# Performance work log

Hardware: AMD Instinct MI355X
Metric: run time of the kernel (lower is better)

Reference implementation:

```python
import jax, jax.numpy as jnp
import numpy as np

B, N, C, H = 8, 4096, 768, 8


def setup_inputs() -> dict:
    key = jax.random.key(0)
    k1, k2, k3 = jax.random.split(key, 3)
    x = jax.random.normal(k1, (B, N, C), dtype=jnp.float32)
    W_qkv = jax.random.normal(k2, (C, 3 * C), dtype=jnp.float32) * 0.02
    W_proj = jax.random.normal(k3, (C, C), dtype=jnp.float32) * 0.02
    b_proj = jnp.zeros((C,), dtype=jnp.float32)
    temp = jnp.ones((H, 1, 1), dtype=jnp.float32)
    return {"x": x, "W_qkv": W_qkv, "W_proj": W_proj, "b_proj": b_proj, "temp": temp}


def reference(x, W_qkv, W_proj, b_proj, temp):
    b, n, c = x.shape
    h = temp.shape[0]
    d = c // h
    # qkv: [B,N,3C] -> [B,N,H,D,3]  (matches tf.reshape split order)
    qkv = (x @ W_qkv).reshape(b, n, h, d, 3)
    q, k, v = qkv[..., 0], qkv[..., 1], qkv[..., 2]
    # L2-normalize along the patch axis (axis=1), as tf.linalg.normalize
    q = q / jnp.linalg.norm(q, axis=1, keepdims=True)
    k = k / jnp.linalg.norm(k, axis=1, keepdims=True)
    # channel-wise (cross-covariance) attention: [B,H,D,D]
    attn = jnp.einsum('bnhd,bnhe->bhde', q, k) * temp
    attn = jax.nn.softmax(attn, axis=-1)
    # apply to v and fold heads back: [B,N,C]
    y = jnp.einsum('bhde,bnhe->bnhd', attn, v).reshape(b, n, c)
    return y @ W_proj + b_proj
```

## Files before the change

kernel.cpp:

```cpp
#include <hip/hip_runtime.h>

typedef __attribute__((ext_vector_type(8))) short short8;
typedef __attribute__((ext_vector_type(4))) float f32x4;

__device__ inline unsigned short f2b(float f) {
  unsigned int u = __builtin_bit_cast(unsigned int, f);
  u = (u + 0x7FFFu + ((u >> 16) & 1u)) >> 16;
  return (unsigned short)u;
}
__device__ inline float b2f(unsigned short s) {
  unsigned int u = ((unsigned int)s) << 16;
  return __builtin_bit_cast(float, u);
}

__device__ inline void async16(const void* g, void* l) {
  __builtin_amdgcn_global_load_lds((__attribute__((address_space(1))) void*)(g),
                                   (__attribute__((address_space(3))) void*)(l), 16, 0, 0);
}

__global__ void cvt_x(const float4* __restrict__ x, ushort4* __restrict__ xb, int n4) {
  int i = blockIdx.x * blockDim.x + threadIdx.x;
  int stride = gridDim.x * blockDim.x;
  for (; i < n4; i += stride) {
    float4 v = x[i];
    ushort4 o;
    o.x = f2b(v.x); o.y = f2b(v.y); o.z = f2b(v.z); o.w = f2b(v.w);
    xb[i] = o;
  }
}

__global__ __launch_bounds__(256) void t_wqkv(const float* __restrict__ W, unsigned short* __restrict__ Wt) {
  __shared__ float tile[32][33];
  int j0 = blockIdx.x * 32, c0 = blockIdx.y * 32;
  int tx = threadIdx.x & 31, ty = threadIdx.x >> 5;
#pragma unroll
  for (int r = 0; r < 32; r += 8)
    tile[ty + r][tx] = W[(size_t)(c0 + ty + r) * 2304 + j0 + tx];
  __syncthreads();
#pragma unroll
  for (int r = 0; r < 32; r += 8) {
    int j = j0 + ty + r;
    int h = j / 288, rem = j - h * 288;
    int d = rem / 3, s = rem - d * 3;
    int jj = s * 768 + h * 96 + d;
    Wt[(size_t)jj * 768 + c0 + tx] = f2b(tile[tx][ty + r]);
  }
}

__global__ __launch_bounds__(256) void t_wproj(const float* __restrict__ W, unsigned short* __restrict__ Wt) {
  __shared__ float tile[32][33];
  int j0 = blockIdx.x * 32, c0 = blockIdx.y * 32;
  int tx = threadIdx.x & 31, ty = threadIdx.x >> 5;
#pragma unroll
  for (int r = 0; r < 32; r += 8)
    tile[ty + r][tx] = W[(size_t)(c0 + ty + r) * 768 + j0 + tx];
  __syncthreads();
#pragma unroll
  for (int r = 0; r < 32; r += 8)
    Wt[(size_t)(j0 + ty + r) * 768 + c0 + tx] = f2b(tile[tx][ty + r]);
}

__global__ __launch_bounds__(512, 2) void gemm_qkv(
    const unsigned short* __restrict__ A, const unsigned short* __restrict__ Bt,
    unsigned short* __restrict__ Q, unsigned short* __restrict__ Kd, unsigned short* __restrict__ V) {
  extern __shared__ __align__(16) unsigned short smem[];
  const int tid = threadIdx.x;
  const int wave = tid >> 6, lane = tid & 63;
  const int mlane = lane & 15, quad = lane >> 4;
  const int m0 = blockIdx.x * 256, n0 = blockIdx.y * 256;
  const int wm = (wave >> 2) * 128;
  const int wn = (wave & 3) * 64;

  f32x4 acc[8][4] = {};

  auto stage = [&](int kt, int c) {
    const int k0 = kt * 64;
    unsigned short* As_c = smem + c * 32768;
    unsigned short* Bs_c = As_c + 16384;
#pragma unroll
    for (int i = 0; i < 4; ++i) {
      int ebase = i * 512 + (wave << 6);
      int e = ebase + lane;
      int row = e >> 3, slot = e & 7;
      async16(A + (size_t)(m0 + row) * 768 + k0 + slot * 8, As_c + (size_t)ebase * 8);
      async16(Bt + (size_t)(n0 + row) * 768 + k0 + slot * 8, Bs_c + (size_t)ebase * 8);
    }
  };

  stage(0, 0);
  stage(1, 1);
  asm volatile("s_waitcnt vmcnt(8)" ::: "memory");
  __builtin_amdgcn_s_barrier();

#pragma unroll 1
  for (int t = 0; t < 12; ++t) {
    const int c = t & 1;
    const unsigned short* As_c = smem + c * 32768;
    const unsigned short* Bs_c = As_c + 16384;

    short8 af[2][2][4];
    short8 bf[2][4];
#pragma unroll
    for (int mh = 0; mh < 2; ++mh)
#pragma unroll
      for (int kk = 0; kk < 2; ++kk)
#pragma unroll
        for (int f = 0; f < 4; ++f)
          af[mh][kk][f] = *(const short8*)&As_c[(wm + mh * 64 + f * 16 + mlane) * 64 + kk * 32 + quad * 8];
#pragma unroll
    for (int kk = 0; kk < 2; ++kk)
#pragma unroll
      for (int j = 0; j < 4; ++j)
        bf[kk][j] = *(const short8*)&Bs_c[(wn + j * 16 + mlane) * 64 + kk * 32 + quad * 8];

    if (t < 10) {
      asm volatile("s_waitcnt lgkmcnt(0)" ::: "memory");
      __builtin_amdgcn_sched_barrier(0);
      __builtin_amdgcn_s_barrier();
      stage(t + 2, c);
    }

    __builtin_amdgcn_s_setprio(1);
#pragma unroll
    for (int kk = 0; kk < 2; ++kk)
#pragma unroll
      for (int mh = 0; mh < 2; ++mh)
#pragma unroll
        for (int f = 0; f < 4; ++f)
#pragma unroll
          for (int j = 0; j < 4; ++j)
            acc[mh * 4 + f][j] =
                __builtin_amdgcn_mfma_f32_16x16x32_bf16(af[mh][kk][f], bf[kk][j], acc[mh * 4 + f][j], 0, 0, 0);
    __builtin_amdgcn_s_setprio(0);

    if (t < 10) {
      asm volatile("s_waitcnt vmcnt(8)" ::: "memory");
      __builtin_amdgcn_s_barrier();
    } else if (t == 10) {
      asm volatile("s_waitcnt vmcnt(0)" ::: "memory");
      __builtin_amdgcn_s_barrier();
    }
  }

  const int bb = m0 >> 12;
  const int nb = (m0 & 4095) + wm + quad * 4;
#pragma unroll
  for (int j = 0; j < 4; ++j) {
    int jj = n0 + wn + j * 16 + mlane;
    int s = jj / 768;
    int hd = jj - s * 768;
    int h = hd / 96;
    int d = hd - h * 96;
    unsigned short* dst = (s == 0) ? Q : (s == 1) ? Kd : V;
    size_t colbase = ((size_t)(bb * 8 + h) * 4096) * 96 + d;
#pragma unroll
    for (int mf = 0; mf < 8; ++mf) {
      int n = nb + (mf >> 2) * 64 + (mf & 3) * 16;
#pragma unroll
      for (int r = 0; r < 4; ++r)
        dst[colbase + (size_t)(n + r) * 96] = f2b(acc[mf][j][r]);
    }
  }
}

__global__ __launch_bounds__(256) void attn_partial(
    const unsigned short* __restrict__ Q, const unsigned short* __restrict__ Kd,
    float* __restrict__ Spart, float* __restrict__ sq, float* __restrict__ sk) {
  int chunk = blockIdx.x;
  int bh = blockIdx.y;
  __shared__ __align__(16) unsigned short QT[96 * 72];
  __shared__ __align__(16) unsigned short KT[96 * 72];
  int t = threadIdx.x;
  int wave = t >> 6, lane = t & 63, mlane = lane & 15, quad = lane >> 4;
  int wrow = (wave >> 1) * 48, wcol = (wave & 1) * 48;
  f32x4 acc[3][3] = {};
  const unsigned int* qp = (const unsigned int*)(Q + (size_t)bh * 4096 * 96);
  const unsigned int* kp = (const unsigned int*)(Kd + (size_t)bh * 4096 * 96);
  int c = t % 48, rg = t / 48;
  int nbeg = chunk * 256;
  float aq0 = 0.f, aq1 = 0.f, ak0 = 0.f, ak1 = 0.f;
  for (int n0 = nbeg; n0 < nbeg + 256; n0 += 64) {
    __syncthreads();
    if (rg < 5) {
      for (int n = rg; n < 64; n += 5) {
        unsigned int qv = qp[(size_t)(n0 + n) * 48 + c];
        unsigned int kv = kp[(size_t)(n0 + n) * 48 + c];
        QT[(2 * c) * 72 + n] = (unsigned short)(qv & 0xffff);
        QT[(2 * c + 1) * 72 + n] = (unsigned short)(qv >> 16);
        KT[(2 * c) * 72 + n] = (unsigned short)(kv & 0xffff);
        KT[(2 * c + 1) * 72 + n] = (unsigned short)(kv >> 16);
        float q0 = b2f((unsigned short)(qv & 0xffff)), q1 = b2f((unsigned short)(qv >> 16));
        float k0 = b2f((unsigned short)(kv & 0xffff)), k1 = b2f((unsigned short)(kv >> 16));
        aq0 += q0 * q0; aq1 += q1 * q1; ak0 += k0 * k0; ak1 += k1 * k1;
      }
    }
    __syncthreads();
#pragma unroll
    for (int kk = 0; kk < 64; kk += 32) {
      short8 a[3], bf[3];
#pragma unroll
      for (int f = 0; f < 3; ++f)
        a[f] = *(const short8*)&QT[(wrow + f * 16 + mlane) * 72 + kk + quad * 8];
#pragma unroll
      for (int f = 0; f < 3; ++f)
        bf[f] = *(const short8*)&KT[(wcol + f * 16 + mlane) * 72 + kk + quad * 8];
#pragma unroll
      for (int i = 0; i < 3; ++i)
#pragma unroll
        for (int j = 0; j < 3; ++j)
          acc[i][j] = __builtin_amdgcn_mfma_f32_16x16x32_bf16(a[i], bf[j], acc[i][j], 0, 0, 0);
    }
  }
  if (rg < 5) {
    atomicAdd(&sq[bh * 96 + 2 * c], aq0);
    atomicAdd(&sq[bh * 96 + 2 * c + 1], aq1);
    atomicAdd(&sk[bh * 96 + 2 * c], ak0);
    atomicAdd(&sk[bh * 96 + 2 * c + 1], ak1);
  }
  float* dst = Spart + ((size_t)bh * 16 + chunk) * 9216;
#pragma unroll
  for (int i = 0; i < 3; ++i)
#pragma unroll
    for (int j = 0; j < 3; ++j)
#pragma unroll
      for (int r = 0; r < 4; ++r)
        dst[(wrow + i * 16 + quad * 4 + r) * 96 + wcol + j * 16 + mlane] = acc[i][j][r];
}

__global__ __launch_bounds__(256) void attn_finalize(
    const float* __restrict__ Spart, const float* __restrict__ sq,
    const float* __restrict__ sk, const float* __restrict__ temp,
    unsigned short* __restrict__ P) {
  int bh = blockIdx.x, h = bh & 7;
  __shared__ float S[9216];
  __shared__ float rk[96], rq[96];
  int t = threadIdx.x;
  const float* base = Spart + (size_t)bh * 16 * 9216;
  if (t < 96) {
    rk[t] = rsqrtf(sk[bh * 96 + t]);
    rq[t] = rsqrtf(sq[bh * 96 + t]) * temp[h];
  }
  __syncthreads();
  for (int i = t; i < 9216; i += 256) {
    float s = 0.f;
#pragma unroll
    for (int c2 = 0; c2 < 16; ++c2) s += base[(size_t)c2 * 9216 + i];
    int d = i / 96, e = i - d * 96;
    S[i] = s * rq[d] * rk[e];
  }
  __syncthreads();
  if (t < 96) {
    int d = t;
    float mx = -1e30f;
    for (int e = 0; e < 96; ++e) mx = fmaxf(mx, S[d * 96 + e]);
    float sum = 0.f;
    for (int e = 0; e < 96; ++e) {
      float v = expf(S[d * 96 + e] - mx);
      S[d * 96 + e] = v;
      sum += v;
    }
    float inv = 1.0f / sum;
    for (int e = 0; e < 96; ++e)
      P[(size_t)bh * 9216 + d * 96 + e] = f2b(S[d * 96 + e] * inv);
  }
}

__global__ __launch_bounds__(256) void gemm_pv(
    const unsigned short* __restrict__ V, const unsigned short* __restrict__ P,
    unsigned short* __restrict__ y) {
  int bh = blockIdx.y;
  int b = bh >> 3, h = bh & 7;
  int m0 = blockIdx.x * 128;
  int t = threadIdx.x, wave = t >> 6, lane = t & 63, mlane = lane & 15, quad = lane >> 4;
  const unsigned short* Vb = V + (size_t)bh * 4096 * 96;
  const unsigned short* Pb = P + (size_t)bh * 9216;
  f32x4 acc[2][6] = {};
#pragma unroll
  for (int kk = 0; kk < 96; kk += 32) {
    short8 a[2], bfr[6];
#pragma unroll
    for (int i = 0; i < 2; ++i)
      a[i] = *(const short8*)&Vb[(size_t)(m0 + wave * 32 + i * 16 + mlane) * 96 + kk + quad * 8];
#pragma unroll
    for (int j = 0; j < 6; ++j)
      bfr[j] = *(const short8*)&Pb[(j * 16 + mlane) * 96 + kk + quad * 8];
#pragma unroll
    for (int i = 0; i < 2; ++i)
#pragma unroll
      for (int j = 0; j < 6; ++j)
        acc[i][j] = __builtin_amdgcn_mfma_f32_16x16x32_bf16(a[i], bfr[j], acc[i][j], 0, 0, 0);
  }
#pragma unroll
  for (int i = 0; i < 2; ++i) {
    int n = m0 + wave * 32 + i * 16 + quad * 4;
#pragma unroll
    for (int j = 0; j < 6; ++j) {
      int d = j * 16 + mlane;
#pragma unroll
      for (int r = 0; r < 4; ++r)
        y[((size_t)b * 4096 + n + r) * 768 + h * 96 + d] = f2b(acc[i][j][r]);
    }
  }
}

__global__ __launch_bounds__(256) void gemm_proj(
    const unsigned short* __restrict__ A, const unsigned short* __restrict__ Bt,
    const float* __restrict__ bias, float* __restrict__ out) {
  __shared__ __align__(16) unsigned short As[128 * 64];
  __shared__ __align__(16) unsigned short Bs[128 * 64];
  const int tid = threadIdx.x;
  const int wave = tid >> 6, lane = tid & 63;
  const int mlane = lane & 15, quad = lane >> 4;
  const int m0 = blockIdx.x * 128, n0 = blockIdx.y * 128;
  const int wm = (wave >> 1) * 64, wn = (wave & 1) * 64;
  f32x4 acc[4][4] = {};
  for (int k0 = 0; k0 < 768; k0 += 64) {
    __syncthreads();
#pragma unroll
    for (int t = 0; t < 4; ++t) {
      int ebase = t * 256 + (wave << 6);
      int e = ebase + lane;
      int row = e >> 3, c8 = e & 7;
      async16(A + (size_t)(m0 + row) * 768 + k0 + c8 * 8, As + ebase * 8);
      async16(Bt + (size_t)(n0 + row) * 768 + k0 + c8 * 8, Bs + ebase * 8);
    }
    __syncthreads();
#pragma unroll
    for (int kk = 0; kk < 64; kk += 32) {
      short8 a[4], b[4];
#pragma unroll
      for (int f = 0; f < 4; ++f)
        a[f] = *(const short8*)&As[(wm + f * 16 + mlane) * 64 + kk + quad * 8];
#pragma unroll
      for (int f = 0; f < 4; ++f)
        b[f] = *(const short8*)&Bs[(wn + f * 16 + mlane) * 64 + kk + quad * 8];
#pragma unroll
      for (int i = 0; i < 4; ++i)
#pragma unroll
        for (int j = 0; j < 4; ++j)
          acc[i][j] = __builtin_amdgcn_mfma_f32_16x16x32_bf16(a[i], b[j], acc[i][j], 0, 0, 0);
    }
  }
#pragma unroll
  for (int fn = 0; fn < 4; ++fn) {
    int col = n0 + wn + fn * 16 + mlane;
    float bv = bias[col];
#pragma unroll
    for (int fm = 0; fm < 4; ++fm) {
      int m = m0 + wm + fm * 16 + quad * 4;
#pragma unroll
      for (int r = 0; r < 4; ++r)
        out[(size_t)(m + r) * 768 + col] = acc[fm][fn][r] + bv;
    }
  }
}

extern "C" void kernel_launch(void* const* d_in, const int* in_sizes, int n_in,
                              void* d_out, int out_size, void* d_ws, size_t ws_size,
                              hipStream_t stream) {
  const float* x = (const float*)d_in[0];
  const float* Wqkv = (const float*)d_in[1];
  const float* Wproj = (const float*)d_in[2];
  const float* bias = (const float*)d_in[3];
  const float* temp = (const float*)d_in[4];
  float* out = (float*)d_out;

  char* ws = (char*)d_ws;
  size_t off = 0;
  auto alloc = [&](size_t bytes) -> void* {
    void* p = ws + off;
    off += (bytes + 255) & ~(size_t)255;
    return p;
  };
  unsigned short* xb = (unsigned short*)alloc(32768ull * 768 * 2);
  unsigned short* Wtq = (unsigned short*)alloc(2304ull * 768 * 2);
  unsigned short* Wtp = (unsigned short*)alloc(768ull * 768 * 2);
  unsigned short* Q = (unsigned short*)alloc(64ull * 4096 * 96 * 2);
  unsigned short* Kd = (unsigned short*)alloc(64ull * 4096 * 96 * 2);
  unsigned short* V = (unsigned short*)alloc(64ull * 4096 * 96 * 2);
  float* sq = (float*)alloc(64 * 96 * 4);
  float* sk = (float*)alloc(64 * 96 * 4);
  unsigned short* P = (unsigned short*)alloc(64ull * 9216 * 2);
  (void)off; (void)ws_size; (void)in_sizes; (void)n_in; (void)out_size;

  float* Spart = out;

  static bool attr_set = false;
  if (!attr_set) {
    hipFuncSetAttribute((const void*)gemm_qkv, hipFuncAttributeMaxDynamicSharedMemorySize, 131072);
    attr_set = true;
  }

  cvt_x<<<4096, 256, 0, stream>>>((const float4*)x, (ushort4*)xb, 32768 * 768 / 4);
  t_wqkv<<<dim3(72, 24), 256, 0, stream>>>(Wqkv, Wtq);
  t_wproj<<<dim3(24, 24), 256, 0, stream>>>(Wproj, Wtp);
  hipMemsetAsync(sq, 0, 64 * 96 * 4, stream);
  hipMemsetAsync(sk, 0, 64 * 96 * 4, stream);
  gemm_qkv<<<dim3(128, 9), 512, 131072, stream>>>(xb, Wtq, Q, Kd, V);
  attn_partial<<<dim3(16, 64), 256, 0, stream>>>(Q, Kd, Spart, sq, sk);
  attn_finalize<<<64, 256, 0, stream>>>(Spart, sq, sk, temp, P);
  gemm_pv<<<dim3(32, 64), 256, 0, stream>>>(V, P, xb );
  gemm_proj<<<dim3(256, 6), 256, 0, stream>>>(xb , Wtp, bias, out);
}
```

Measured before the change: 552.3 us.

## Swizzle LDS tiles and interleave fragment loads with MFMA in QKV GEMM

The QKV GEMM now stores A and B tiles in LDS with an XOR swizzle on the 16-byte slot index, which is meant to remove bank conflicts on the fragment reads. The main loop is split into four phases, each loading a subset of fragments and then issuing 16 MFMAs, with barriers in between. This lowers register pressure and lets LDS reads overlap with other waves' math. The next-stage prefetch is issued before the last MFMA phase, and the epilogue store loop is reordered. The extra barriers add sync overhead.

```diff
diff --git a/kernel.cpp b/kernel.cpp
--- a/kernel.cpp
+++ b/kernel.cpp
@@ -68,97 +68,140 @@
   const int wave = tid >> 6, lane = tid & 63;
   const int mlane = lane & 15, quad = lane >> 4;
   const int m0 = blockIdx.x * 256, n0 = blockIdx.y * 256;
-  const int wm = (wave >> 2) * 128;
+  const int ah = wave >> 2;
+  const int wm = ah * 128;
   const int wn = (wave & 3) * 64;
+  const int bh = wn >> 7;
+  const int bl = wn & 64;
 
   f32x4 acc[8][4] = {};
 
   auto stage = [&](int kt, int c) {
     const int k0 = kt * 64;
-    unsigned short* As_c = smem + c * 32768;
-    unsigned short* Bs_c = As_c + 16384;
-#pragma unroll
-    for (int i = 0; i < 4; ++i) {
-      int ebase = i * 512 + (wave << 6);
-      int e = ebase + lane;
-      int row = e >> 3, slot = e & 7;
-      async16(A + (size_t)(m0 + row) * 768 + k0 + slot * 8, As_c + (size_t)ebase * 8);
-      async16(Bt + (size_t)(n0 + row) * 768 + k0 + slot * 8, Bs_c + (size_t)ebase * 8);
-    }
+#pragma unroll
+    for (int h = 0; h < 4; ++h) {
+      const unsigned short* src = (h < 2) ? A : Bt;
+      const int rbase = ((h < 2) ? m0 : n0) + (h & 1) * 128;
+      unsigned short* ldsbase = smem + c * 32768 + h * 8192;
+#pragma unroll
+      for (int i = 0; i < 2; ++i) {
+        int ebase = i * 512 + (wave << 6);
+        int e = ebase + lane;
+        int row = e >> 3;
+        int slot = (e & 7) ^ (row & 7);
+        async16(src + (size_t)(rbase + row) * 768 + k0 + slot * 8, ldsbase + ebase * 8);
+      }
+    }
+  };
+
+  auto rdA = [&](const unsigned short* base, int mh, int kk, int f) -> short8 {
+    int r = mh * 64 + f * 16 + mlane;
+    return *(const short8*)&base[r * 64 + ((kk * 32 + quad * 8) ^ ((r & 7) << 3))];
+  };
+  auto rdB = [&](const unsigned short* base, int kk, int j) -> short8 {
+    int r = bl + j * 16 + mlane;
+    return *(const short8*)&base[r * 64 + ((kk * 32 + quad * 8) ^ ((r & 7) << 3))];
   };
 
   stage(0, 0);
   stage(1, 1);
   asm volatile("s_waitcnt vmcnt(8)" ::: "memory");
+  __builtin_amdgcn_sched_barrier(0);
   __builtin_amdgcn_s_barrier();
 
 #pragma unroll 1
   for (int t = 0; t < 12; ++t) {
     const int c = t & 1;
-    const unsigned short* As_c = smem + c * 32768;
-    const unsigned short* Bs_c = As_c + 16384;
-
-    short8 af[2][2][4];
-    short8 bf[2][4];
-#pragma unroll
-    for (int mh = 0; mh < 2; ++mh)
-#pragma unroll
-      for (int kk = 0; kk < 2; ++kk)
-#pragma unroll
-        for (int f = 0; f < 4; ++f)
-          af[mh][kk][f] = *(const short8*)&As_c[(wm + mh * 64 + f * 16 + mlane) * 64 + kk * 32 + quad * 8];
-#pragma unroll
-    for (int kk = 0; kk < 2; ++kk)
+    const unsigned short* Abase = smem + c * 32768 + ah * 8192;
+    const unsigned short* Bbase = smem + c * 32768 + 16384 + bh * 8192;
+    short8 a0[4], a1[4], b0[4], b1[4];
+
+#pragma unroll
+    for (int j = 0; j < 4; ++j) b0[j] = rdB(Bbase, 0, j);
+#pragma unroll
+    for (int f = 0; f < 4; ++f) a0[f] = rdA(Abase, 0, 0, f);
+    asm volatile("s_waitcnt lgkmcnt(0)" ::: "memory");
+    __builtin_amdgcn_sched_barrier(0);
+    __builtin_amdgcn_s_setprio(1);
+#pragma unroll
+    for (int f = 0; f < 4; ++f)
 #pragma unroll
       for (int j = 0; j < 4; ++j)
-        bf[kk][j] = *(const short8*)&Bs_c[(wn + j * 16 + mlane) * 64 + kk * 32 + quad * 8];
-
-    if (t < 10) {
-      asm volatile("s_waitcnt lgkmcnt(0)" ::: "memory");
-      __builtin_amdgcn_sched_barrier(0);
-      __builtin_amdgcn_s_barrier();
-      stage(t + 2, c);
-    }
-
+        acc[f][j] = __builtin_amdgcn_mfma_f32_16x16x32_bf16(a0[f], b0[j], acc[f][j], 0, 0, 0);
+    __builtin_amdgcn_s_setprio(0);
+    __builtin_amdgcn_s_barrier();
+
+#pragma unroll
+    for (int f = 0; f < 4; ++f) a1[f] = rdA(Abase, 1, 0, f);
+#pragma unroll
+    for (int j = 0; j < 4; ++j) b1[j] = rdB(Bbase, 1, j);
+    asm volatile("s_waitcnt lgkmcnt(0)" ::: "memory");
+    __builtin_amdgcn_sched_barrier(0);
     __builtin_amdgcn_s_setprio(1);
 #pragma unroll
-    for (int kk = 0; kk < 2; ++kk)
-#pragma unroll
-      for (int mh = 0; mh < 2; ++mh)
-#pragma unroll
-        for (int f = 0; f < 4; ++f)
-#pragma unroll
-          for (int j = 0; j < 4; ++j)
-            acc[mh * 4 + f][j] =
-                __builtin_amdgcn_mfma_f32_16x16x32_bf16(af[mh][kk][f], bf[kk][j], acc[mh * 4 + f][j], 0, 0, 0);
+    for (int f = 0; f < 4; ++f)
+#pragma unroll
+      for (int j = 0; j < 4; ++j)
+        acc[4 + f][j] = __builtin_amdgcn_mfma_f32_16x16x32_bf16(a1[f], b0[j], acc[4 + f][j], 0, 0, 0);
     __builtin_amdgcn_s_setprio(0);
-
+    __builtin_amdgcn_s_barrier();
+
+#pragma unroll
+    for (int f = 0; f < 4; ++f) a0[f] = rdA(Abase, 0, 1, f);
+#pragma unroll
+    for (int f = 0; f < 4; ++f) a1[f] = rdA(Abase, 1, 1, f);
+    asm volatile("s_waitcnt lgkmcnt(0)" ::: "memory");
+    __builtin_amdgcn_sched_barrier(0);
+    __builtin_amdgcn_s_setprio(1);
+#pragma unroll
+    for (int f = 0; f < 4; ++f)
+#pragma unroll
+      for (int j = 0; j < 4; ++j)
+        acc[f][j] = __builtin_amdgcn_mfma_f32_16x16x32_bf16(a0[f], b1[j], acc[f][j], 0, 0, 0);
+    __builtin_amdgcn_s_setprio(0);
+    __builtin_amdgcn_s_barrier();
+
+    if (t < 10) stage(t + 2, c);
+    __builtin_amdgcn_s_setprio(1);
+#pragma unroll
+    for (int f = 0; f < 4; ++f)
+#pragma unroll
+      for (int j = 0; j < 4; ++j)
+        acc[4 + f][j] = __builtin_amdgcn_mfma_f32_16x16x32_bf16(a1[f], b1[j], acc[4 + f][j], 0, 0, 0);
+    __builtin_amdgcn_s_setprio(0);
     if (t < 10) {
       asm volatile("s_waitcnt vmcnt(8)" ::: "memory");
+      __builtin_amdgcn_sched_barrier(0);
       __builtin_amdgcn_s_barrier();
     } else if (t == 10) {
       asm volatile("s_waitcnt vmcnt(0)" ::: "memory");
+      __builtin_amdgcn_sched_barrier(0);
       __builtin_amdgcn_s_barrier();
     }
   }
 
   const int bb = m0 >> 12;
-  const int nb = (m0 & 4095) + wm + quad * 4;
+  const int nbase = (m0 & 4095) + wm + quad * 4;
+  unsigned short* dstp[4];
+  size_t cb[4];
 #pragma unroll
   for (int j = 0; j < 4; ++j) {
     int jj = n0 + wn + j * 16 + mlane;
-    int s = jj / 768;
+    int s = (jj >= 1536) ? 2 : (jj >= 768) ? 1 : 0;
     int hd = jj - s * 768;
     int h = hd / 96;
     int d = hd - h * 96;
-    unsigned short* dst = (s == 0) ? Q : (s == 1) ? Kd : V;
-    size_t colbase = ((size_t)(bb * 8 + h) * 4096) * 96 + d;
-#pragma unroll
-    for (int mf = 0; mf < 8; ++mf) {
-      int n = nb + (mf >> 2) * 64 + (mf & 3) * 16;
-#pragma unroll
-      for (int r = 0; r < 4; ++r)
-        dst[colbase + (size_t)(n + r) * 96] = f2b(acc[mf][j][r]);
+    dstp[j] = (s == 0) ? Q : (s == 1) ? Kd : V;
+    cb[j] = ((size_t)(bb * 8 + h) * 4096) * 96 + d;
+  }
+#pragma unroll
+  for (int mf = 0; mf < 8; ++mf) {
+    int n = nbase + (mf >> 2) * 64 + (mf & 3) * 16;
+#pragma unroll
+    for (int r = 0; r < 4; ++r) {
+#pragma unroll
+      for (int j = 0; j < 4; ++j)
+        dstp[j][cb[j] + (size_t)(n + r) * 96] = f2b(acc[mf][j][r]);
     }
   }
 }
```

After: 490.0 us. -11.3%, faster.
